# Kernel optimization log

Measured on AMD Instinct MI355X. Metric: run time of the kernel, lower is better.

Reference implementation:

```python
import jax, jax.numpy as jnp
import numpy as np
from jax import lax

L = 6        # n_layers
C = 192      # hidden_channels
FC = 768     # filter_channels
H = 2        # n_heads
DK = C // H  # k_channels per head
K = 3        # ffn kernel_size
W = 4        # window_size
B = 4
T = 2048
EPS = 1e-5


def setup_inputs() -> dict:
    key = jax.random.key(0)
    ks = jax.random.split(key, 16)
    def rn(k, shape, scale):
        return jax.random.normal(k, shape, dtype=jnp.float32) * scale
    xavier = (2.0 / (C + C)) ** 0.5
    return {
        "x": jax.random.normal(ks[0], (B, C, T), dtype=jnp.float32),
        "x_mask": jnp.ones((B, 1, T), dtype=jnp.float32),
        "wq": rn(ks[1], (L, C, C), xavier), "bq": jnp.zeros((L, C), jnp.float32),
        "wk": rn(ks[2], (L, C, C), xavier), "bk": jnp.zeros((L, C), jnp.float32),
        "wv": rn(ks[3], (L, C, C), xavier), "bv": jnp.zeros((L, C), jnp.float32),
        "wo": rn(ks[4], (L, C, C), xavier), "bo": jnp.zeros((L, C), jnp.float32),
        "rel_k": rn(ks[5], (L, 1, 2 * W + 1, DK), DK ** -0.5),
        "rel_v": rn(ks[6], (L, 1, 2 * W + 1, DK), DK ** -0.5),
        "ln1_g": jnp.ones((L, C), jnp.float32), "ln1_b": jnp.zeros((L, C), jnp.float32),
        "ffn_w1": rn(ks[7], (L, FC, C, K), 0.02), "ffn_b1": jnp.zeros((L, FC), jnp.float32),
        "ffn_w2": rn(ks[8], (L, C, FC, K), 0.02), "ffn_b2": jnp.zeros((L, C), jnp.float32),
        "ln2_g": jnp.ones((L, C), jnp.float32), "ln2_b": jnp.zeros((L, C), jnp.float32),
    }


def _layer_norm_ch(x, g, b):
    # normalize over channel dim (axis=1) of [B, C, T]
    m = jnp.mean(x, axis=1, keepdims=True)
    v = jnp.mean((x - m) ** 2, axis=1, keepdims=True)
    return g[None, :, None] * (x - m) * lax.rsqrt(v + EPS) + b[None, :, None]


def _conv1x1(x, w, b):
    return jnp.einsum('oc,bct->bot', w, x) + b[None, :, None]


def _conv1d(x, w, b, pad):
    y = lax.conv_general_dilated(x, w, window_strides=(1,), padding=[(pad, pad)],
                                 dimension_numbers=('NCH', 'OIH', 'NCH'))
    return y + b[None, :, None]


def _get_rel(emb, length):
    # emb: [1, 2W+1, DK] -> [1, 2*length-1, DK]
    pad_len = max(length - (W + 1), 0)
    start = max(W + 1 - length, 0)
    emb = jnp.pad(emb, ((0, 0), (pad_len, pad_len), (0, 0)))
    return emb[:, start:start + 2 * length - 1]


def _rel_to_abs(x):
    # [B, H, L, 2L-1] -> [B, H, L, L]
    b, h, l, _ = x.shape
    x = jnp.pad(x, ((0, 0), (0, 0), (0, 0), (0, 1)))
    x = x.reshape(b, h, l * 2 * l)
    x = jnp.pad(x, ((0, 0), (0, 0), (0, l - 1)))
    return x.reshape(b, h, l + 1, 2 * l - 1)[:, :, :l, l - 1:]


def _abs_to_rel(x):
    # [B, H, L, L] -> [B, H, L, 2L-1]
    b, h, l, _ = x.shape
    x = jnp.pad(x, ((0, 0), (0, 0), (0, 0), (0, l - 1)))
    x = x.reshape(b, h, l * (2 * l - 1))
    x = jnp.pad(x, ((0, 0), (0, 0), (l, 0)))
    return x.reshape(b, h, l, 2 * l)[:, :, :, 1:]


def reference(x, x_mask, wq, bq, wk, bk, wv, bv, wo, bo, rel_k, rel_v,
              ln1_g, ln1_b, ffn_w1, ffn_b1, ffn_w2, ffn_b2, ln2_g, ln2_b):
    attn_mask = x_mask[:, :, None, :] * x_mask[:, :, :, None]  # [B,1,T,T]
    x = x * x_mask
    scale = DK ** -0.5
    pad = (K - 1) // 2
    for l in range(L):
        residual = x
        q = _conv1x1(x, wq[l], bq[l]).reshape(B, H, DK, T).transpose(0, 1, 3, 2)
        k = _conv1x1(x, wk[l], bk[l]).reshape(B, H, DK, T).transpose(0, 1, 3, 2)
        v = _conv1x1(x, wv[l], bv[l]).reshape(B, H, DK, T).transpose(0, 1, 3, 2)
        qs = q * scale
        scores = jnp.einsum('bhtd,bhsd->bhts', qs, k)
        rk = _get_rel(rel_k[l], T)[0]  # [2T-1, DK], heads shared
        scores = scores + _rel_to_abs(jnp.einsum('bhtd,md->bhtm', qs, rk))
        scores = jnp.where(attn_mask == 0, jnp.float32(-1e4), scores)
        p = jax.nn.softmax(scores, axis=-1)
        out = jnp.einsum('bhts,bhsd->bhtd', p, v)
        rv = _get_rel(rel_v[l], T)[0]
        out = out + jnp.einsum('bhtm,md->bhtd', _abs_to_rel(p), rv)
        out = out.transpose(0, 1, 3, 2).reshape(B, C, T)
        out = _conv1x1(out, wo[l], bo[l])
        x = _layer_norm_ch(residual + out, ln1_g[l], ln1_b[l])
        residual = x
        h = _conv1d(x * x_mask, ffn_w1[l], ffn_b1[l], pad)
        h = jax.nn.relu(h)  # activation != 'gelu'
        h = _conv1d(h, ffn_w2[l], ffn_b2[l], pad)
        h = h * x_mask
        x = _layer_norm_ch(residual + h, ln2_g[l], ln2_b[l])
    return x * x_mask
```

## Files before the change

### kernel.cpp

```cpp
#include <hip/hip_runtime.h>

#define LNUM 6
#define CH 192
#define FCH 768
#define NH 2
#define DKH 96
#define WIN 4
#define BATCH 4
#define TLEN 2048
#define EPSV 1e-5f
#define SCH 4
#define CHUNK (TLEN / SCH)
#define NBCT (BATCH*CH*TLEN)
#define NBFT (BATCH*FCH*TLEN)
#define BHT (BATCH*NH*TLEN)

typedef __attribute__((ext_vector_type(8))) short bf16x8;
typedef __attribute__((ext_vector_type(4))) float f32x4;
typedef __attribute__((ext_vector_type(8))) unsigned short u16x8;

__device__ __forceinline__ unsigned short f2bf(float f) {
  unsigned int u = __builtin_bit_cast(unsigned int, f);
  u = (u + 0x7fffu + ((u >> 16) & 1u)) >> 16;
  return (unsigned short)u;
}
__device__ __forceinline__ float bf2f(unsigned short s) {
  return __builtin_bit_cast(float, ((unsigned int)s) << 16);
}
__device__ __forceinline__ float exp2a(float x) {
#if __has_builtin(__builtin_amdgcn_exp2f)
  return __builtin_amdgcn_exp2f(x);
#else
  return exp2f(x);
#endif
}

__global__ __launch_bounds__(256) void prep_all(
    const float* __restrict__ wq, const float* __restrict__ wk, const float* __restrict__ wv,
    const float* __restrict__ bq, const float* __restrict__ bk, const float* __restrict__ bv,
    const float* __restrict__ wo, const float* __restrict__ fw1, const float* __restrict__ fw2,
    unsigned short* __restrict__ Wqkv, float* __restrict__ Bqkv,
    unsigned short* __restrict__ Wob, unsigned short* __restrict__ W1b,
    unsigned short* __restrict__ W2b)
{
  const float qscale = 0.10206207261596575f * 1.4426950408889634f;
  const int n0 = LNUM * 576 * CH;
  const int n1 = LNUM * CH * CH;
  const int n2 = LNUM * 3 * FCH * CH;
  const int n3 = LNUM * 3 * CH * FCH;
  int total = n0 + n1 + n2 + n3;
  for (int i = blockIdx.x * 256 + threadIdx.x; i < total; i += gridDim.x * 256) {
    if (i < n0) {
      int c = i % CH; int n = (i / CH) % 576; int l = i / (CH * 576);
      float sc = (n < 192) ? qscale : 1.f;
      const float* src = (n < 192) ? wq : (n < 384) ? wk : wv;
      int nn = n % 192;
      Wqkv[i] = f2bf(src[((size_t)l * CH + nn) * CH + c] * sc);
      if (c == 0) {
        const float* bs = (n < 192) ? bq : (n < 384) ? bk : bv;
        Bqkv[l * 576 + n] = bs[l * CH + nn] * sc;
      }
    } else if (i < n0 + n1) {
      int j = i - n0;
      Wob[j] = f2bf(wo[j]);
    } else if (i < n0 + n1 + n2) {
      int j = i - n0 - n1;
      int c = j % CH; int t1 = j / CH;
      int f = t1 % FCH; int t2 = t1 / FCH;
      int kk = t2 % 3; int l = t2 / 3;
      W1b[j] = f2bf(fw1[(((size_t)l * FCH + f) * CH + c) * 3 + kk]);
    } else {
      int j = i - n0 - n1 - n2;
      int c = j % FCH; int t1 = j / FCH;
      int f = t1 % CH; int t2 = t1 / CH;
      int kk = t2 % 3; int l = t2 / 3;
      W2b[j] = f2bf(fw2[(((size_t)l * CH + f) * FCH + c) * 3 + kk]);
    }
  }
}

__global__ __launch_bounds__(256) void tin_kernel(const float* __restrict__ x,
    const float* __restrict__ mask, float* __restrict__ Xc, unsigned short* __restrict__ Xbf) {
  __shared__ float ls[32][33];
  int b = blockIdx.z; int c0 = blockIdx.y * 32, t0 = blockIdx.x * 32;
  int tx = threadIdx.x & 31, ty = threadIdx.x >> 5;
  #pragma unroll
  for (int j = 0; j < 4; ++j)
    ls[ty + j * 8][tx] = x[((size_t)b * CH + c0 + ty + j * 8) * TLEN + t0 + tx];
  __syncthreads();
  #pragma unroll
  for (int j = 0; j < 4; ++j) {
    int t = t0 + ty + j * 8;
    float v = ls[tx][ty + j * 8] * mask[b * TLEN + t];
    size_t o = ((size_t)b * TLEN + t) * CH + c0 + tx;
    Xc[o] = v; Xbf[o] = f2bf(v);
  }
}

__global__ __launch_bounds__(256) void tout_kernel(const float* __restrict__ Xc,
    const float* __restrict__ mask, float* __restrict__ out) {
  __shared__ float ls[32][33];
  int b = blockIdx.z; int c0 = blockIdx.y * 32, t0 = blockIdx.x * 32;
  int tx = threadIdx.x & 31, ty = threadIdx.x >> 5;
  #pragma unroll
  for (int j = 0; j < 4; ++j)
    ls[ty + j * 8][tx] = Xc[((size_t)b * TLEN + t0 + ty + j * 8) * CH + c0 + tx];
  __syncthreads();
  #pragma unroll
  for (int j = 0; j < 4; ++j)
    out[((size_t)b * CH + c0 + ty + j * 8) * TLEN + t0 + tx] =
        ls[tx][ty + j * 8] * mask[b * TLEN + t0 + tx];
}

template<int OUTMODE, int NSHIFT, int RELU, int KSPLIT, int MFR>
__global__ __launch_bounds__(256) void gemm_tc(
    const unsigned short* __restrict__ A, const unsigned short* __restrict__ Bw,
    const float* __restrict__ bias, void* __restrict__ Y, int Cin, int N)
{
  constexpr int HALO = (NSHIFT == 3) ? 1 : 0;
  constexpr int AROWS = MFR * 32 + 2 * HALO;
  constexpr int ACH = (AROWS * 8 + 255) / 256;
  constexpr int BCH = (NSHIFT * 64 * 8) / 256;
  __shared__ __align__(16) unsigned short As[AROWS][72];
  __shared__ __align__(16) unsigned short Bs[NSHIFT][64][72];
  int zz = blockIdx.z;
  int b = zz / KSPLIT, ks = zz % KSPLIT;
  int t0 = blockIdx.x * (MFR * 32), n0 = blockIdx.y * 64;
  int tid = threadIdx.x;
  int w = tid >> 6, lane = tid & 63;
  int wr = w >> 1, wc = w & 1;
  int lr = lane & 15, lg = lane >> 4;
  const unsigned short* Ab = A + (size_t)b * TLEN * Cin;
  int klen = Cin / KSPLIT, k0 = ks * klen;

  int ar[ACH], ac8[ACH]; bool aok[ACH], ain[ACH];
  #pragma unroll
  for (int j = 0; j < ACH; ++j) {
    int f = tid + j * 256;
    ar[j] = f >> 3; ac8[j] = (f & 7) * 8;
    aok[j] = (f < AROWS * 8);
    int tg = t0 - HALO + ar[j];
    ain[j] = aok[j] && (!HALO || (tg >= 0 && tg < TLEN));
  }
  int brr[BCH], bkk[BCH], bc8[BCH];
  #pragma unroll
  for (int j = 0; j < BCH; ++j) {
    int f = tid + j * 256;
    bkk[j] = f >> 9; brr[j] = (f >> 3) & 63; bc8[j] = (f & 7) * 8;
  }

  u16x8 areg[ACH], breg[BCH];
  f32x4 acc[MFR][2] = {};

  #pragma unroll
  for (int j = 0; j < ACH; ++j) {
    u16x8 v = {};
    if (ain[j]) v = *(const u16x8*)&Ab[(size_t)(t0 - HALO + ar[j]) * Cin + k0 + ac8[j]];
    areg[j] = v;
  }
  #pragma unroll
  for (int j = 0; j < BCH; ++j)
    breg[j] = *(const u16x8*)&Bw[((size_t)bkk[j] * N + n0 + brr[j]) * Cin + k0 + bc8[j]];

  for (int kc = k0; kc < k0 + klen; kc += 64) {
    __syncthreads();
    #pragma unroll
    for (int j = 0; j < ACH; ++j)
      if (aok[j]) *(u16x8*)&As[ar[j]][ac8[j]] = areg[j];
    #pragma unroll
    for (int j = 0; j < BCH; ++j)
      *(u16x8*)&Bs[bkk[j]][brr[j]][bc8[j]] = breg[j];
    if (kc + 64 < k0 + klen) {
      int kn = kc + 64;
      #pragma unroll
      for (int j = 0; j < ACH; ++j) {
        u16x8 v = {};
        if (ain[j]) v = *(const u16x8*)&Ab[(size_t)(t0 - HALO + ar[j]) * Cin + kn + ac8[j]];
        areg[j] = v;
      }
      #pragma unroll
      for (int j = 0; j < BCH; ++j)
        breg[j] = *(const u16x8*)&Bw[((size_t)bkk[j] * N + n0 + brr[j]) * Cin + kn + bc8[j]];
    }
    __syncthreads();
    #pragma unroll
    for (int kk = 0; kk < NSHIFT; ++kk) {
      #pragma unroll
      for (int k2 = 0; k2 < 2; ++k2) {
        bf16x8 b0 = *(const bf16x8*)&Bs[kk][wc * 32 + lr][k2 * 32 + lg * 8];
        bf16x8 b1 = *(const bf16x8*)&Bs[kk][wc * 32 + 16 + lr][k2 * 32 + lg * 8];
        #pragma unroll
        for (int i = 0; i < MFR; ++i) {
          bf16x8 a = *(const bf16x8*)&As[wr * MFR * 16 + i * 16 + lr + kk][k2 * 32 + lg * 8];
          acc[i][0] = __builtin_amdgcn_mfma_f32_16x16x32_bf16(a, b0, acc[i][0], 0, 0, 0);
          acc[i][1] = __builtin_amdgcn_mfma_f32_16x16x32_bf16(a, b1, acc[i][1], 0, 0, 0);
        }
      }
    }
  }
  #pragma unroll
  for (int i = 0; i < MFR; ++i) {
    #pragma unroll
    for (int j = 0; j < 2; ++j) {
      int n = n0 + wc * 32 + j * 16 + lr;
      float bb = (ks == 0) ? bias[n] : 0.f;
      float vals[4];
      #pragma unroll
      for (int r = 0; r < 4; ++r) {
        float v = acc[i][j][r] + bb;
        if (RELU) v = fmaxf(v, 0.f);
        vals[r] = v;
      }
      int trow = t0 + wr * MFR * 16 + i * 16 + lg * 4;
      if (OUTMODE == 0) {
        unsigned short* Yp = (unsigned short*)Y + ((size_t)b * TLEN + trow) * N + n;
        #pragma unroll
        for (int r = 0; r < 4; ++r) Yp[(size_t)r * N] = f2bf(vals[r]);
      } else {
        unsigned short* base = (unsigned short*)Y;
        if (n0 < 192) {
          unsigned short* Yp = base + ((size_t)b * TLEN + trow) * CH + n;
          #pragma unroll
          for (int r = 0; r < 4; ++r) Yp[(size_t)r * CH] = f2bf(vals[r]);
        } else if (n0 < 384) {
          unsigned short* Yp = base + (size_t)NBCT + ((size_t)b * TLEN + trow) * CH + (n - 192);
          #pragma unroll
          for (int r = 0; r < 4; ++r) Yp[(size_t)r * CH] = f2bf(vals[r]);
        } else {
          ushort4 pk;
          pk.x = f2bf(vals[0]); pk.y = f2bf(vals[1]); pk.z = f2bf(vals[2]); pk.w = f2bf(vals[3]);
          *(ushort4*)(base + 2 * (size_t)NBCT + ((size_t)b * CH + (n - 384)) * TLEN + trow) = pk;
        }
      }
    }
  }
}

__global__ __launch_bounds__(256) void gemm_wolnc(
    const unsigned short* __restrict__ Opart, const float* __restrict__ mG,
    const float* __restrict__ lG, const float* __restrict__ bandG,
    const float* __restrict__ relv,
    const unsigned short* __restrict__ Bw, const float* __restrict__ bias,
    const float* __restrict__ g, const float* __restrict__ bt,
    float* __restrict__ Xc, unsigned short* __restrict__ Xbf)
{
  __shared__ __align__(16) unsigned short Af[16][200];
  __shared__ __align__(16) unsigned short Bs[192][72];
  __shared__ float sred[4][16][2];
  __shared__ float ce[16][2][4];
  __shared__ float cinvL[16][2];
  __shared__ float cbx[16][2][9];
  __shared__ float relvS[9 * 96];
  int b = blockIdx.y;
  int t0 = blockIdx.x * 16;
  int tid = threadIdx.x;
  int w = tid >> 6, lane = tid & 63;
  int lr = lane & 15, lg = lane >> 4;
  int brr[6], bc8[6];
  #pragma unroll
  for (int j = 0; j < 6; ++j) { int f = tid + j * 256; brr[j] = f >> 3; bc8[j] = (f & 7) * 8; }

  u16x8 breg[6];
  #pragma unroll
  for (int j = 0; j < 6; ++j)
    breg[j] = *(const u16x8*)&Bw[(size_t)brr[j] * CH + bc8[j]];

  for (int f = tid; f < 864; f += 256) relvS[f] = relv[f];
  if (tid < 32) {
    int r = tid >> 1, h = tid & 1;
    int t = t0 + r;
    size_t grow = (size_t)(b * 2 + h) * TLEN + t;
    float mv[SCH], lv[SCH], m = -1e30f;
    #pragma unroll
    for (int c = 0; c < SCH; ++c) {
      mv[c] = mG[(size_t)c * BHT + grow];
      lv[c] = lG[(size_t)c * BHT + grow];
      m = fmaxf(m, mv[c]);
    }
    float L = 0.f;
    #pragma unroll
    for (int c = 0; c < SCH; ++c) {
      float e = exp2a(mv[c] - m);
      ce[r][h][c] = e; L += lv[c] * e;
    }
    cinvL[r][h] = 1.f / L;
    #pragma unroll
    for (int dd = 0; dd < 9; ++dd) {
      int s = t + dd - WIN;
      cbx[r][h][dd] = (s >= 0 && s < TLEN) ? exp2a(bandG[grow * 9 + dd] - m) : 0.f;
    }
  }
  __syncthreads();
  #pragma unroll
  for (int j = 0; j < 12; ++j) {
    int f = tid + j * 256;
    int row = f / 192, col = f - row * 192;
    int h = (col >= 96) ? 1 : 0, d = col - h * 96;
    size_t grow = (size_t)(b * 2 + h) * TLEN + t0 + row;
    float acc = 0.f;
    #pragma unroll
    for (int c = 0; c < SCH; ++c)
      acc += bf2f(Opart[((size_t)c * BHT + grow) * 96 + d]) * ce[row][h][c];
    #pragma unroll
    for (int dd = 0; dd < 9; ++dd)
      acc += cbx[row][h][dd] * relvS[dd * 96 + d];
    Af[row][col] = f2bf(acc * cinvL[row][h]);
  }

  f32x4 acc3[3] = {};
  for (int kc = 0; kc < CH; kc += 64) {
    __syncthreads();
    #pragma unroll
    for (int j = 0; j < 6; ++j) *(u16x8*)&Bs[brr[j]][bc8[j]] = breg[j];
    if (kc + 64 < CH) {
      int kn = kc + 64;
      #pragma unroll
      for (int j = 0; j < 6; ++j)
        breg[j] = *(const u16x8*)&Bw[(size_t)brr[j] * CH + kn + bc8[j]];
    }
    __syncthreads();
    #pragma unroll
    for (int k2 = 0; k2 < 2; ++k2) {
      bf16x8 a = *(const bf16x8*)&Af[lr][kc + k2 * 32 + lg * 8];
      #pragma unroll
      for (int j = 0; j < 3; ++j) {
        bf16x8 bfr = *(const bf16x8*)&Bs[w * 48 + j * 16 + lr][k2 * 32 + lg * 8];
        acc3[j] = __builtin_amdgcn_mfma_f32_16x16x32_bf16(a, bfr, acc3[j], 0, 0, 0);
      }
    }
  }
  float vv[3][4], sp[4] = {}, sp2[4] = {};
  #pragma unroll
  for (int j = 0; j < 3; ++j) {
    int col = w * 48 + j * 16 + lr;
    float bb = bias[col];
    #pragma unroll
    for (int r = 0; r < 4; ++r) {
      int row = t0 + lg * 4 + r;
      float y = acc3[j][r] + bb;
      float res = Xc[((size_t)b * TLEN + row) * CH + col];
      float t = res + y;
      vv[j][r] = t; sp[r] += t; sp2[r] += t * t;
    }
  }
  #pragma unroll
  for (int m = 1; m <= 8; m <<= 1)
    #pragma unroll
    for (int r = 0; r < 4; ++r) {
      sp[r] += __shfl_xor(sp[r], m, 64);
      sp2[r] += __shfl_xor(sp2[r], m, 64);
    }
  __syncthreads();
  if (lr == 0) {
    #pragma unroll
    for (int r = 0; r < 4; ++r) {
      sred[w][lg * 4 + r][0] = sp[r];
      sred[w][lg * 4 + r][1] = sp2[r];
    }
  }
  __syncthreads();
  #pragma unroll
  for (int r = 0; r < 4; ++r) {
    int row = lg * 4 + r;
    float s  = sred[0][row][0] + sred[1][row][0] + sred[2][row][0] + sred[3][row][0];
    float s2 = sred[0][row][1] + sred[1][row][1] + sred[2][row][1] + sred[3][row][1];
    float mean = s * (1.f / CH);
    float var = s2 * (1.f / CH) - mean * mean;
    float rs = rsqrtf(var + EPSV);
    #pragma unroll
    for (int j = 0; j < 3; ++j) {
      int col = w * 48 + j * 16 + lr;
      float o = g[col] * (vv[j][r] - mean) * rs + bt[col];
      size_t idx = ((size_t)b * TLEN + t0 + row) * CH + col;
      Xc[idx] = o; Xbf[idx] = f2bf(o);
    }
  }
}

__global__ __launch_bounds__(256) void ln_cl_kernel(
    const float* __restrict__ res, const unsigned short* __restrict__ yb,
    const float* __restrict__ g, const float* __restrict__ bt,
    float* __restrict__ Xc, unsigned short* __restrict__ Xbf)
{
  int row = blockIdx.x * 4 + (threadIdx.x >> 6);
  int lane = threadIdx.x & 63;
  const float* r = res + (size_t)row * CH;
  const unsigned short* y = yb + (size_t)row * CH;
  float v[3]; float s = 0.f, s2 = 0.f;
  #pragma unroll
  for (int j = 0; j < 3; ++j) {
    float t = r[lane + 64 * j] + bf2f(y[lane + 64 * j]);
    v[j] = t; s += t; s2 += t * t;
  }
  #pragma unroll
  for (int m = 1; m <= 32; m <<= 1) {
    s += __shfl_xor(s, m, 64);
    s2 += __shfl_xor(s2, m, 64);
  }
  float mean = s * (1.f / CH);
  float var = s2 * (1.f / CH) - mean * mean;
  float rs = rsqrtf(var + EPSV);
  #pragma unroll
  for (int j = 0; j < 3; ++j) {
    int c = lane + 64 * j;
    float o = g[c] * (v[j] - mean) * rs + bt[c];
    size_t idx = (size_t)row * CH + c;
    Xc[idx] = o; Xbf[idx] = f2bf(o);
  }
}

__global__ __launch_bounds__(256, 4) void flash_part(
    const unsigned short* __restrict__ Qg, const unsigned short* __restrict__ Kg,
    const unsigned short* __restrict__ Vg, const float* __restrict__ relk,
    unsigned short* __restrict__ Opart, float* __restrict__ mG, float* __restrict__ lG,
    float* __restrict__ bandG)
{
  __shared__ __align__(16) unsigned short KsB[64 * 104];
  __shared__ __align__(16) unsigned short QV[96 * 72];
  __shared__ float qrk[64][9];
  int id = blockIdx.x;
  int bh = id & 7;
  int rest = id >> 3;
  int t0 = (rest & 31) * 64;
  int zc = rest >> 5;
  int c0 = zc * CHUNK;
  int b = bh >> 1, h = bh & 1;
  int tid = threadIdx.x; int w = tid >> 6, lane = tid & 63;
  int lr = lane & 15, lg = lane >> 4;
  int q = w * 16 + lr;
  const unsigned short* Qb = Qg + (size_t)b * TLEN * CH + h * DKH;
  const unsigned short* Kb = Kg + (size_t)b * TLEN * CH + h * DKH;
  const unsigned short* Vb = Vg + ((size_t)b * CH + h * DKH) * TLEN;
  unsigned short (*Qs)[104] = (unsigned short(*)[104])QV;
  unsigned short (*Vs)[72] = (unsigned short(*)[72])QV;
  unsigned short (*Ks)[104] = (unsigned short(*)[104])KsB;
  unsigned short (*Ps)[72] = (unsigned short(*)[72])KsB;

  int kr[3], kc8[3], vr[3], vc8[3];
  #pragma unroll
  for (int j = 0; j < 3; ++j) {
    int f = tid + j * 256;
    kr[j] = f / 12; kc8[j] = (f % 12) * 8;
    vr[j] = f >> 3; vc8[j] = (f & 7) * 8;
  }

  for (int f = tid; f < 64 * 12; f += 256) {
    int r = f / 12, c8 = (f % 12) * 8;
    *(u16x8*)&Qs[r][c8] = *(const u16x8*)&Qb[(size_t)(t0 + r) * CH + c8];
  }
  __syncthreads();
  bool overlap = (t0 + 64 + WIN > c0) && (t0 - WIN < c0 + CHUNK);
  if (overlap) {
    for (int f = tid; f < 576; f += 256) {
      int r = f / 9, dd = f - (f / 9) * 9;
      float s = 0.f;
      #pragma unroll 8
      for (int d = 0; d < DKH; ++d) s += bf2f(Qs[r][d]) * relk[dd * DKH + d];
      qrk[r][dd] = s;
    }
  }
  bf16x8 qf[3];
  #pragma unroll
  for (int kc = 0; kc < 3; ++kc) qf[kc] = *(const bf16x8*)&Qs[q][kc * 32 + lg * 8];
  float mrow = -1e30f, lrow = 0.f;
  f32x4 oacc[6] = {};

  u16x8 kreg[3], vreg[3];
  #pragma unroll
  for (int j = 0; j < 3; ++j)
    kreg[j] = *(const u16x8*)&Kb[(size_t)(c0 + kr[j]) * CH + kc8[j]];
  #pragma unroll
  for (int j = 0; j < 3; ++j)
    vreg[j] = *(const u16x8*)&Vb[(size_t)vr[j] * TLEN + c0 + vc8[j]];

  for (int it = 0; it < CHUNK / 64; ++it) {
    int s0 = c0 + it * 64;
    __syncthreads();
    #pragma unroll
    for (int j = 0; j < 3; ++j) *(u16x8*)&Ks[kr[j]][kc8[j]] = kreg[j];
    #pragma unroll
    for (int j = 0; j < 3; ++j) *(u16x8*)&Vs[vr[j]][vc8[j]] = vreg[j];
    if (it + 1 < CHUNK / 64) {
      int sn = s0 + 64;
      #pragma unroll
      for (int j = 0; j < 3; ++j)
        kreg[j] = *(const u16x8*)&Kb[(size_t)(sn + kr[j]) * CH + kc8[j]];
      #pragma unroll
      for (int j = 0; j < 3; ++j)
        vreg[j] = *(const u16x8*)&Vb[(size_t)vr[j] * TLEN + sn + vc8[j]];
    }
    __syncthreads();

    f32x4 sacc[4] = {};
    __builtin_amdgcn_s_setprio(1);
    #pragma unroll
    for (int kc = 0; kc < 3; ++kc) {
      #pragma unroll
      for (int ct = 0; ct < 4; ++ct) {
        bf16x8 kfr = *(const bf16x8*)&Ks[ct * 16 + lr][kc * 32 + lg * 8];
        sacc[ct] = __builtin_amdgcn_mfma_f32_16x16x32_bf16(kfr, qf[kc], sacc[ct], 0, 0, 0);
      }
    }
    __builtin_amdgcn_s_setprio(0);
    if (s0 + 64 + WIN > t0 && s0 < t0 + 64 + WIN) {
      #pragma unroll
      for (int ct = 0; ct < 4; ++ct)
        #pragma unroll
        for (int r = 0; r < 4; ++r) {
          int dlt = (s0 + ct * 16 + lg * 4 + r) - (t0 + q);
          if (dlt >= -WIN && dlt <= WIN) {
            float v = sacc[ct][r] + qrk[q][dlt + WIN];
            sacc[ct][r] = v;
            bandG[((size_t)bh * TLEN + t0 + q) * 9 + dlt + WIN] = v;
          }
        }
    }
    float cm[4];
    #pragma unroll
    for (int ct = 0; ct < 4; ++ct)
      cm[ct] = fmaxf(fmaxf(sacc[ct][0], sacc[ct][1]), fmaxf(sacc[ct][2], sacc[ct][3]));
    float tmax = fmaxf(fmaxf(cm[0], cm[1]), fmaxf(cm[2], cm[3]));
    tmax = fmaxf(tmax, __shfl_xor(tmax, 16, 64));
    tmax = fmaxf(tmax, __shfl_xor(tmax, 32, 64));
    bool upd = !__all(tmax <= mrow + 8.f);
    float mnew = upd ? fmaxf(mrow, tmax) : mrow;
    float psum = 0.f;
    ushort4 pk[4];
    #pragma unroll
    for (int ct = 0; ct < 4; ++ct) {
      float p0 = exp2a(sacc[ct][0] - mnew), p1 = exp2a(sacc[ct][1] - mnew);
      float p2 = exp2a(sacc[ct][2] - mnew), p3 = exp2a(sacc[ct][3] - mnew);
      psum += (p0 + p1) + (p2 + p3);
      pk[ct].x = f2bf(p0); pk[ct].y = f2bf(p1); pk[ct].z = f2bf(p2); pk[ct].w = f2bf(p3);
    }
    if (upd) {
      float alpha = exp2a(mrow - mnew);
      lrow *= alpha;
      float alo[4];
      #pragma unroll
      for (int r = 0; r < 4; ++r) alo[r] = __shfl(alpha, lg * 4 + r, 64);
      #pragma unroll
      for (int dt = 0; dt < 6; ++dt)
        #pragma unroll
        for (int r = 0; r < 4; ++r) oacc[dt][r] *= alo[r];
      mrow = mnew;
    }
    lrow += psum;
    __syncthreads();
    #pragma unroll
    for (int ct = 0; ct < 4; ++ct)
      *(ushort4*)&Ps[q][ct * 16 + lg * 4] = pk[ct];
    __builtin_amdgcn_s_setprio(1);
    #pragma unroll
    for (int ks = 0; ks < 2; ++ks) {
      bf16x8 pa = *(const bf16x8*)&Ps[q][ks * 32 + lg * 8];
      #pragma unroll
      for (int dt = 0; dt < 6; ++dt) {
        bf16x8 vf = *(const bf16x8*)&Vs[dt * 16 + lr][ks * 32 + lg * 8];
        oacc[dt] = __builtin_amdgcn_mfma_f32_16x16x32_bf16(pa, vf, oacc[dt], 0, 0, 0);
      }
    }
    __builtin_amdgcn_s_setprio(0);
  }

  size_t pbase = ((size_t)zc * (BATCH * NH) + bh) * TLEN + t0;
  #pragma unroll
  for (int dt = 0; dt < 6; ++dt)
    #pragma unroll
    for (int r = 0; r < 4; ++r)
      Opart[(pbase + w * 16 + lg * 4 + r) * 96 + dt * 16 + lr] = f2bf(oacc[dt][r]);
  float lfull = lrow;
  lfull += __shfl_xor(lfull, 16, 64);
  lfull += __shfl_xor(lfull, 32, 64);
  if (lg == 0) {
    mG[pbase + q] = mrow;
    lG[pbase + q] = lfull;
  }
}

extern "C" void kernel_launch(void* const* d_in, const int* in_sizes, int n_in,
                              void* d_out, int out_size, void* d_ws, size_t ws_size,
                              hipStream_t stream) {
  (void)in_sizes; (void)n_in; (void)out_size; (void)ws_size;
  const float* x    = (const float*)d_in[0];
  const float* mask = (const float*)d_in[1];
  const float* wq   = (const float*)d_in[2];
  const float* bq   = (const float*)d_in[3];
  const float* wk   = (const float*)d_in[4];
  const float* bk   = (const float*)d_in[5];
  const float* wv   = (const float*)d_in[6];
  const float* bv   = (const float*)d_in[7];
  const float* wo   = (const float*)d_in[8];
  const float* bo   = (const float*)d_in[9];
  const float* relk = (const float*)d_in[10];
  const float* relv = (const float*)d_in[11];
  const float* ln1g = (const float*)d_in[12];
  const float* ln1b = (const float*)d_in[13];
  const float* fw1  = (const float*)d_in[14];
  const float* fb1  = (const float*)d_in[15];
  const float* fw2  = (const float*)d_in[16];
  const float* fb2  = (const float*)d_in[17];
  const float* ln2g = (const float*)d_in[18];
  const float* ln2b = (const float*)d_in[19];

  char* p = (char*)d_ws;
  float* Xc = (float*)p;                      p += (size_t)NBCT * 4;
  unsigned short* Xbf  = (unsigned short*)p;  p += (size_t)NBCT * 2;
  unsigned short* Qbf  = (unsigned short*)p;  p += (size_t)NBCT * 2;
  unsigned short* Kbf  = (unsigned short*)p;  p += (size_t)NBCT * 2;
  unsigned short* Vbf  = (unsigned short*)p;  p += (size_t)NBCT * 2;
  char* R = p;                                p += (size_t)NBCT * 16;
  unsigned short* Opart = (unsigned short*)R;
  unsigned short* Ybf = (unsigned short*)R;
  unsigned short* Hbf = (unsigned short*)(R + (size_t)NBCT * 2);
  float* mG = (float*)p;                      p += (size_t)SCH * BHT * 4;
  float* lG = (float*)p;                      p += (size_t)SCH * BHT * 4;
  float* bandG = (float*)p;                   p += (size_t)BHT * 9 * 4;
  unsigned short* Wqkv = (unsigned short*)p;  p += (size_t)LNUM * 576 * CH * 2;
  float* Bqkv = (float*)p;                    p += (size_t)LNUM * 576 * 4;
  unsigned short* Wob  = (unsigned short*)p;  p += (size_t)LNUM * CH * CH * 2;
  unsigned short* W1b  = (unsigned short*)p;  p += (size_t)LNUM * 3 * FCH * CH * 2;
  unsigned short* W2b  = (unsigned short*)p;

  prep_all<<<2048, 256, 0, stream>>>(wq, wk, wv, bq, bk, bv, wo, fw1, fw2,
                                     Wqkv, Bqkv, Wob, W1b, W2b);
  tin_kernel<<<dim3(TLEN / 32, CH / 32, BATCH), 256, 0, stream>>>(x, mask, Xc, Xbf);

  for (int l = 0; l < LNUM; ++l) {
    gemm_tc<3, 1, 0, 1, 2><<<dim3(32, 9, 4), 256, 0, stream>>>(
        Xbf, Wqkv + (size_t)l * 576 * CH, Bqkv + l * 576, Qbf, CH, 576);
    flash_part<<<dim3(32 * 8 * SCH), 256, 0, stream>>>(
        Qbf, Kbf, Vbf, relk + (size_t)l * 9 * DKH, Opart, mG, lG, bandG);
    gemm_wolnc<<<dim3(TLEN / 16, BATCH), 256, 0, stream>>>(
        Opart, mG, lG, bandG, relv + (size_t)l * 9 * DKH,
        Wob + (size_t)l * CH * CH, bo + l * CH,
        ln1g + l * CH, ln1b + l * CH, Xc, Xbf);
    gemm_tc<0, 3, 1, 1, 2><<<dim3(32, 12, 4), 256, 0, stream>>>(
        Xbf, W1b + (size_t)l * 3 * FCH * CH, fb1 + l * FCH, Hbf, CH, FCH);
    gemm_tc<0, 3, 0, 1, 2><<<dim3(32, 3, 4), 256, 0, stream>>>(
        Hbf, W2b + (size_t)l * 3 * CH * FCH, fb2 + l * CH, Ybf, FCH, CH);
    ln_cl_kernel<<<BATCH * TLEN / 4, 256, 0, stream>>>(
        Xc, Ybf, ln2g + l * CH, ln2b + l * CH, Xc, Xbf);
  }
  tout_kernel<<<dim3(TLEN / 32, CH / 32, BATCH), 256, 0, stream>>>(Xc, mask, (float*)d_out);
}
```

Before: 593.5 us.

## Fuse FFN second conv GEMM with residual add and LayerNorm

Replaces the second FFN conv GEMM plus the separate LayerNorm kernel with one kernel. Each block computes a 32-row by all-192-channel tile, so the LayerNorm over channels can be reduced in-block and applied before writing. This removes the bf16 Y round trip and one launch per layer. In exchange the grid shrinks to 256 blocks, each with a longer K loop over 768x3 and register prefetch, which may underfill the GPU.

New measurement: 597.2 us. No clear change (+0.6%).

```diff
diff --git a/kernel.cpp b/kernel.cpp
--- a/kernel.cpp
+++ b/kernel.cpp
@@ -377,36 +377,140 @@
   }
 }
 
-__global__ __launch_bounds__(256) void ln_cl_kernel(
-    const float* __restrict__ res, const unsigned short* __restrict__ yb,
-    const float* __restrict__ g, const float* __restrict__ bt,
-    float* __restrict__ Xc, unsigned short* __restrict__ Xbf)
+__global__ __launch_bounds__(256) void gemm_f2lnc(
+    const unsigned short* __restrict__ A, const unsigned short* __restrict__ Bw,
+    const float* __restrict__ bias, const float* __restrict__ g,
+    const float* __restrict__ bt, float* __restrict__ Xc, unsigned short* __restrict__ Xbf)
 {
-  int row = blockIdx.x * 4 + (threadIdx.x >> 6);
-  int lane = threadIdx.x & 63;
-  const float* r = res + (size_t)row * CH;
-  const unsigned short* y = yb + (size_t)row * CH;
-  float v[3]; float s = 0.f, s2 = 0.f;
-  #pragma unroll
-  for (int j = 0; j < 3; ++j) {
-    float t = r[lane + 64 * j] + bf2f(y[lane + 64 * j]);
-    v[j] = t; s += t; s2 += t * t;
-  }
-  #pragma unroll
-  for (int m = 1; m <= 32; m <<= 1) {
-    s += __shfl_xor(s, m, 64);
-    s2 += __shfl_xor(s2, m, 64);
-  }
-  float mean = s * (1.f / CH);
-  float var = s2 * (1.f / CH) - mean * mean;
-  float rs = rsqrtf(var + EPSV);
-  #pragma unroll
-  for (int j = 0; j < 3; ++j) {
-    int c = lane + 64 * j;
-    float o = g[c] * (v[j] - mean) * rs + bt[c];
-    size_t idx = (size_t)row * CH + c;
-    Xc[idx] = o; Xbf[idx] = f2bf(o);
-  }
+  __shared__ __align__(16) unsigned short As[34][72];
+  __shared__ __align__(16) unsigned short Bs[192][72];
+  __shared__ float sred[4][32][2];
+  int b = blockIdx.y;
+  int t0 = blockIdx.x * 32;
+  int tid = threadIdx.x;
+  int w = tid >> 6, lane = tid & 63;
+  int lr = lane & 15, lg = lane >> 4;
+  const unsigned short* Ab = A + (size_t)b * TLEN * FCH;
+  int ar[2], ac8[2]; bool aok[2], ain[2];
+  #pragma unroll
+  for (int j = 0; j < 2; ++j) {
+    int f = tid + j * 256;
+    ar[j] = f >> 3; ac8[j] = (f & 7) * 8;
+    aok[j] = f < 272;
+    int tg = t0 - 1 + ar[j];
+    ain[j] = aok[j] && tg >= 0 && tg < TLEN;
+  }
+  int brr[6], bc8[6];
+  #pragma unroll
+  for (int j = 0; j < 6; ++j) { int f = tid + j * 256; brr[j] = f >> 3; bc8[j] = (f & 7) * 8; }
+
+  u16x8 areg[2], breg[6];
+  f32x4 acc[2][3] = {};
+  #pragma unroll
+  for (int j = 0; j < 2; ++j) {
+    u16x8 v = {};
+    if (ain[j]) v = *(const u16x8*)&Ab[(size_t)(t0 - 1 + ar[j]) * FCH + ac8[j]];
+    areg[j] = v;
+  }
+  #pragma unroll
+  for (int j = 0; j < 6; ++j)
+    breg[j] = *(const u16x8*)&Bw[(size_t)brr[j] * FCH + bc8[j]];
+
+  for (int kc = 0; kc < FCH; kc += 64) {
+    for (int kk = 0; kk < 3; ++kk) {
+      __syncthreads();
+      if (kk == 0) {
+        #pragma unroll
+        for (int j = 0; j < 2; ++j)
+          if (aok[j]) *(u16x8*)&As[ar[j]][ac8[j]] = areg[j];
+      }
+      #pragma unroll
+      for (int j = 0; j < 6; ++j) *(u16x8*)&Bs[brr[j]][bc8[j]] = breg[j];
+      bool last = (kk == 2) && (kc + 64 >= FCH);
+      if (!last) {
+        int nkk = (kk == 2) ? 0 : kk + 1;
+        int nkc = (kk == 2) ? kc + 64 : kc;
+        #pragma unroll
+        for (int j = 0; j < 6; ++j)
+          breg[j] = *(const u16x8*)&Bw[((size_t)nkk * CH + brr[j]) * FCH + nkc + bc8[j]];
+        if (kk == 2) {
+          #pragma unroll
+          for (int j = 0; j < 2; ++j) {
+            u16x8 v = {};
+            if (ain[j]) v = *(const u16x8*)&Ab[(size_t)(t0 - 1 + ar[j]) * FCH + nkc + ac8[j]];
+            areg[j] = v;
+          }
+        }
+      }
+      __syncthreads();
+      #pragma unroll
+      for (int k2 = 0; k2 < 2; ++k2) {
+        #pragma unroll
+        for (int rf = 0; rf < 2; ++rf) {
+          bf16x8 a = *(const bf16x8*)&As[rf * 16 + lr + kk][k2 * 32 + lg * 8];
+          #pragma unroll
+          for (int j = 0; j < 3; ++j) {
+            bf16x8 bfr = *(const bf16x8*)&Bs[w * 48 + j * 16 + lr][k2 * 32 + lg * 8];
+            acc[rf][j] = __builtin_amdgcn_mfma_f32_16x16x32_bf16(a, bfr, acc[rf][j], 0, 0, 0);
+          }
+        }
+      }
+    }
+  }
+  float vv[2][3][4], sp[2][4] = {}, sp2[2][4] = {};
+  #pragma unroll
+  for (int rf = 0; rf < 2; ++rf)
+    #pragma unroll
+    for (int j = 0; j < 3; ++j) {
+      int col = w * 48 + j * 16 + lr;
+      float bb = bias[col];
+      #pragma unroll
+      for (int r = 0; r < 4; ++r) {
+        int row = t0 + rf * 16 + lg * 4 + r;
+        float y = acc[rf][j][r] + bb;
+        float res = Xc[((size_t)b * TLEN + row) * CH + col];
+        float t = res + y;
+        vv[rf][j][r] = t; sp[rf][r] += t; sp2[rf][r] += t * t;
+      }
+    }
+  #pragma unroll
+  for (int m = 1; m <= 8; m <<= 1)
+    #pragma unroll
+    for (int rf = 0; rf < 2; ++rf)
+      #pragma unroll
+      for (int r = 0; r < 4; ++r) {
+        sp[rf][r] += __shfl_xor(sp[rf][r], m, 64);
+        sp2[rf][r] += __shfl_xor(sp2[rf][r], m, 64);
+      }
+  __syncthreads();
+  if (lr == 0) {
+    #pragma unroll
+    for (int rf = 0; rf < 2; ++rf)
+      #pragma unroll
+      for (int r = 0; r < 4; ++r) {
+        sred[w][rf * 16 + lg * 4 + r][0] = sp[rf][r];
+        sred[w][rf * 16 + lg * 4 + r][1] = sp2[rf][r];
+      }
+  }
+  __syncthreads();
+  #pragma unroll
+  for (int rf = 0; rf < 2; ++rf)
+    #pragma unroll
+    for (int r = 0; r < 4; ++r) {
+      int row = rf * 16 + lg * 4 + r;
+      float s  = sred[0][row][0] + sred[1][row][0] + sred[2][row][0] + sred[3][row][0];
+      float s2 = sred[0][row][1] + sred[1][row][1] + sred[2][row][1] + sred[3][row][1];
+      float mean = s * (1.f / CH);
+      float var = s2 * (1.f / CH) - mean * mean;
+      float rs = rsqrtf(var + EPSV);
+      #pragma unroll
+      for (int j = 0; j < 3; ++j) {
+        int col = w * 48 + j * 16 + lr;
+        float o = g[col] * (vv[rf][j][r] - mean) * rs + bt[col];
+        size_t idx = ((size_t)b * TLEN + t0 + row) * CH + col;
+        Xc[idx] = o; Xbf[idx] = f2bf(o);
+      }
+    }
 }
 
 __global__ __launch_bounds__(256, 4) void flash_part(
@@ -611,7 +715,6 @@
   unsigned short* Vbf  = (unsigned short*)p;  p += (size_t)NBCT * 2;
   char* R = p;                                p += (size_t)NBCT * 16;
   unsigned short* Opart = (unsigned short*)R;
-  unsigned short* Ybf = (unsigned short*)R;
   unsigned short* Hbf = (unsigned short*)(R + (size_t)NBCT * 2);
   float* mG = (float*)p;                      p += (size_t)SCH * BHT * 4;
   float* lG = (float*)p;                      p += (size_t)SCH * BHT * 4;
@@ -637,10 +740,9 @@
         ln1g + l * CH, ln1b + l * CH, Xc, Xbf);
     gemm_tc<0, 3, 1, 1, 2><<<dim3(32, 12, 4), 256, 0, stream>>>(
         Xbf, W1b + (size_t)l * 3 * FCH * CH, fb1 + l * FCH, Hbf, CH, FCH);
-    gemm_tc<0, 3, 0, 1, 2><<<dim3(32, 3, 4), 256, 0, stream>>>(
-        Hbf, W2b + (size_t)l * 3 * CH * FCH, fb2 + l * CH, Ybf, FCH, CH);
-    ln_cl_kernel<<<BATCH * TLEN / 4, 256, 0, stream>>>(
-        Xc, Ybf, ln2g + l * CH, ln2b + l * CH, Xc, Xbf);
+    gemm_f2lnc<<<dim3(TLEN / 32, BATCH), 256, 0, stream>>>(
+        Hbf, W2b + (size_t)l * 3 * CH * FCH, fb2 + l * CH,
+        ln2g + l * CH, ln2b + l * CH, Xc, Xbf);
   }
   tout_kernel<<<dim3(TLEN / 32, CH / 32, BATCH), 256, 0, stream>>>(Xc, mask, (float*)d_out);
 }
```
